# Kernel tuning notes

Measured on AMD Instinct MI355X. Metric: run time of the kernel, lower is better.

Reference implementation:

```python
import jax, jax.numpy as jnp
import numpy as np

STUDENT_TEMP = 0.1
CENTER_MOMENTUM = 0.9
N_CROPS = 8
GLOBAL_CROPS = 2
TOPK = 8
WARMUP_TEACHER_TEMP = 0.04
TEACHER_TEMP = 0.07
WARMUP_EPOCHS = 30
NEPOCHS = 100
B = 256          # per-crop batch
D = 8192         # out_dim


def setup_inputs() -> dict:
    key = jax.random.key(0)
    k1, k2, k3, k4 = jax.random.split(key, 4)
    return {
        "student_output": jax.random.normal(k1, (N_CROPS * B, D), jnp.float32),
        "teacher_output": jax.random.normal(k2, (GLOBAL_CROPS * B, D), jnp.float32),
        "predictor_table": 0.02 * jax.random.normal(k3, (D, D), jnp.float32),
        "center": 0.1 * jax.random.normal(k4, (1, D), jnp.float32),
        "epoch": 35,
    }


def reference(student_output, teacher_output, predictor_table, center, epoch):
    # teacher temperature schedule (static, epoch is a Python int)
    temps = np.concatenate([
        np.linspace(WARMUP_TEACHER_TEMP, TEACHER_TEMP, WARMUP_EPOCHS),
        np.ones(NEPOCHS - WARMUP_EPOCHS) * TEACHER_TEMP,
    ])
    temp = float(temps[epoch])

    # student/teacher softmaxes, chunked per crop
    student_probs = jax.nn.softmax(student_output / STUDENT_TEMP, axis=-1)
    s_chunks = jnp.split(student_probs, N_CROPS, axis=0)          # n_crops x [B, D]
    teacher_probs = jax.nn.softmax((teacher_output - center) / temp, axis=-1)
    t_chunks = jnp.split(teacher_probs, GLOBAL_CROPS, axis=0)     # global_crops x [B, D]

    # pairwise topk-weighted cross entropy
    total_loss = jnp.float32(0.0)
    n_loss_terms = 0
    for iq in range(GLOBAL_CROPS):
        for v in range(N_CROPS):
            if v <= iq:
                continue
            s = t_chunks[iq]                                       # [B, D] teacher probs
            f = s_chunks[v]                                        # [B, D] student probs
            p, indices = jax.lax.top_k(s, TOPK)                    # [B, K]
            p = p / jnp.sum(p, axis=-1, keepdims=True)
            pred = predictor_table[indices] / STUDENT_TEMP         # [B, K, D] gather
            logp = jax.nn.log_softmax(pred, axis=-1)               # [B, K, D]
            # -sum_k sum_d p[b,k] * f[b,d] * logp[b,k,d]  (outer-product weighting)
            loss_b = -jnp.einsum('bk,bd,bkd->b', p, f, logp)
            total_loss = total_loss + loss_b.mean()
            n_loss_terms += 1
    total_loss = total_loss / n_loss_terms

    # EMA center update (no-grad in original; world_size = 1)
    t_ng = jax.lax.stop_gradient(teacher_output)
    batch_center = jnp.mean(t_ng, axis=0, keepdims=True)           # [1, D]
    new_center = center * CENTER_MOMENTUM + batch_center * (1.0 - CENTER_MOMENTUM)

    log_sm_center = jax.nn.log_softmax(center, axis=-1)
    true_entropy = jnp.sum(jax.nn.softmax(center, axis=-1) * log_sm_center, axis=-1)
    entropy = jnp.sum(jax.nn.softmax(batch_center, axis=-1) * log_sm_center, axis=-1)

    return (total_loss, entropy, true_entropy, new_center)
```

## Files before the change

### kernel.cpp

```cpp
#include <hip/hip_runtime.h>
#include <hip/hip_bf16.h>
#include <math.h>

#define D 8192
#define NT 256

__device__ __forceinline__ float wave_sum(float v) {
    #pragma unroll
    for (int o = 32; o > 0; o >>= 1) v += __shfl_xor(v, o, 64);
    return v;
}

__global__ __launch_bounds__(NT) void k_topk(
    const float* __restrict__ teacher, const float* __restrict__ center,
    const int* __restrict__ epoch_p,
    int* __restrict__ idx_ws, float* __restrict__ p_ws, float* __restrict__ out)
{
    const int row = blockIdx.x;
    const int t = threadIdx.x;
    const int lane = t & 63, w = t >> 6;
    __shared__ float svv[8][4];
    __shared__ int   sii[8][4];

    if (row == 0 && t == 0) out[0] = 0.f;

    const int e = epoch_p[0];
    const float temp = (e < 30) ? (0.04f + 0.03f * (float)e / 29.0f) : 0.07f;

    float z[32];
    const float* trow = teacher + (size_t)row * D;
    #pragma unroll
    for (int i = 0; i < 8; ++i) {
        const int d = i * 1024 + t * 4;
        float4 tv = *(const float4*)(trow + d);
        float4 cv = *(const float4*)(center + d);
        z[i*4+0] = tv.x - cv.x; z[i*4+1] = tv.y - cv.y;
        z[i*4+2] = tv.z - cv.z; z[i*4+3] = tv.w - cv.w;
    }

    float mvl = -INFINITY; int mil = 0;
    #pragma unroll
    for (int i = 0; i < 32; ++i)
        if (z[i] > mvl) { mvl = z[i]; mil = i; }

    float topv[8]; int topd[8];
    #pragma unroll 1
    for (int k = 0; k < 8; ++k) {
        float mv = mvl;
        int md = ((mil >> 2) << 10) + t * 4 + (mil & 3);
        #pragma unroll
        for (int o = 32; o > 0; o >>= 1) {
            float ov = __shfl_xor(mv, o, 64);
            int   od = __shfl_xor(md, o, 64);
            if (ov > mv) { mv = ov; md = od; }
        }
        if (lane == 0) { svv[k][w] = mv; sii[k][w] = md; }
        __syncthreads();
        float gv = svv[k][0]; int gd = sii[k][0];
        #pragma unroll
        for (int j = 1; j < 4; ++j)
            if (svv[k][j] > gv) { gv = svv[k][j]; gd = sii[k][j]; }
        topv[k] = gv; topd[k] = gd;
        if (((gd & 1023) >> 2) == t) {
            z[((gd >> 10) << 2) | (gd & 3)] = -INFINITY;
            mvl = -INFINITY; mil = 0;
            #pragma unroll
            for (int i = 0; i < 32; ++i)
                if (z[i] > mvl) { mvl = z[i]; mil = i; }
        }
    }

    if (t == 0) {
        float wgt[8]; float norm = 0.f;
        #pragma unroll
        for (int k = 0; k < 8; ++k) { wgt[k] = __expf((topv[k] - topv[0]) / temp); norm += wgt[k]; }
        const float invn = 1.0f / norm;
        #pragma unroll
        for (int k = 0; k < 8; ++k) {
            p_ws[row * 8 + k] = wgt[k] * invn;
            idx_ws[row * 8 + k] = topd[k];
        }
    }
}

__global__ __launch_bounds__(NT) void k_gather_colsum(
    const float* __restrict__ pred, const int* __restrict__ idx_ws,
    const float* __restrict__ p_ws, const float* __restrict__ teacher,
    float* __restrict__ g_ws, float* __restrict__ part_lse, float* __restrict__ part)
{
    const int bid = blockIdx.x;
    const int t = threadIdx.x;

    if (bid < 128) {
        const int rc = bid >> 3, dc = bid & 7;
        const int d0 = dc * 1024 + t * 4;
        const float* base = teacher + (size_t)rc * 32 * D + d0;
        float4 acc = make_float4(0.f, 0.f, 0.f, 0.f);
        #pragma unroll 4
        for (int r = 0; r < 32; ++r) {
            float4 x = *(const float4*)(base + (size_t)r * D);
            acc.x += x.x; acc.y += x.y; acc.z += x.z; acc.w += x.w;
        }
        *(float4*)(part + (size_t)rc * D + d0) = acc;
        return;
    }

    const int gb  = bid - 128;
    const int row = gb >> 2;
    const int ch  = gb & 3;
    const int lane = t & 63, w = t >> 6;
    const int d0 = ch * 2048 + t * 4;
    __shared__ float sred[4][8];

    int jk[8]; float pk[8];
    #pragma unroll
    for (int k = 0; k < 8; ++k) {
        jk[k] = idx_ws[row * 8 + k];
        pk[k] = p_ws[row * 8 + k];
    }

    float4 a0 = make_float4(0.f,0.f,0.f,0.f), a1 = make_float4(0.f,0.f,0.f,0.f);
    float se[8];
    #pragma unroll
    for (int k = 0; k < 8; ++k) {
        const float* prow = pred + (size_t)jk[k] * D;
        float4 x0 = *(const float4*)(prow + d0);
        float4 x1 = *(const float4*)(prow + d0 + 1024);
        se[k] = __expf(x0.x*10.f) + __expf(x0.y*10.f) + __expf(x0.z*10.f) + __expf(x0.w*10.f)
              + __expf(x1.x*10.f) + __expf(x1.y*10.f) + __expf(x1.z*10.f) + __expf(x1.w*10.f);
        const float p = pk[k];
        a0.x += p*x0.x; a0.y += p*x0.y; a0.z += p*x0.z; a0.w += p*x0.w;
        a1.x += p*x1.x; a1.y += p*x1.y; a1.z += p*x1.z; a1.w += p*x1.w;
    }
    float* grow = g_ws + (size_t)row * D;
    *(float4*)(grow + d0)        = a0;
    *(float4*)(grow + d0 + 1024) = a1;

    #pragma unroll
    for (int k = 0; k < 8; ++k) se[k] = wave_sum(se[k]);
    if (lane == 0) {
        #pragma unroll
        for (int k = 0; k < 8; ++k) sred[w][k] = se[k];
    }
    __syncthreads();
    if (t < 8)
        part_lse[(size_t)gb * 8 + t] =
            sred[0][t] + sred[1][t] + sred[2][t] + sred[3][t];
}

__global__ __launch_bounds__(NT) void k_main(
    const float* __restrict__ student, const float* __restrict__ g_ws,
    const float* __restrict__ p_ws, const float* __restrict__ part_lse,
    const float* __restrict__ part, const float* __restrict__ center,
    float* __restrict__ out)
{
    const int bid = blockIdx.x;
    const int t = threadIdx.x;
    const int lane = t & 63, w = t >> 6;

    if (bid < 2) {
        __shared__ float sm4[4];
        const int r = (bid << 8) | t;
        float c = 0.f;
        #pragma unroll
        for (int k = 0; k < 8; ++k) {
            float s = part_lse[(size_t)(r*4+0)*8+k] + part_lse[(size_t)(r*4+1)*8+k]
                    + part_lse[(size_t)(r*4+2)*8+k] + part_lse[(size_t)(r*4+3)*8+k];
            c += p_ws[r * 8 + k] * __logf(s);
        }
        const float wgt = (bid == 0) ? 7.0f : 6.0f;
        float vv = wave_sum(c * wgt * (1.0f / 3328.0f));
        if (lane == 0) sm4[w] = vv;
        __syncthreads();
        if (t == 0) atomicAdd(out, sm4[0] + sm4[1] + sm4[2] + sm4[3]);
        return;
    }

    if (bid == 2) {
        __shared__ float sm4[4];
        float c[32], bc[32];
        #pragma unroll
        for (int i = 0; i < 8; ++i) {
            const int d = i * 1024 + t * 4;
            float4 cv = *(const float4*)(center + d);
            float4 s = make_float4(0.f, 0.f, 0.f, 0.f);
            for (int rc = 0; rc < 16; ++rc) {
                float4 p = *(const float4*)(part + (size_t)rc * D + d);
                s.x += p.x; s.y += p.y; s.z += p.z; s.w += p.w;
            }
            const float sc = 1.0f / 512.0f;
            bc[i*4+0] = s.x * sc; bc[i*4+1] = s.y * sc;
            bc[i*4+2] = s.z * sc; bc[i*4+3] = s.w * sc;
            c[i*4+0] = cv.x; c[i*4+1] = cv.y; c[i*4+2] = cv.z; c[i*4+3] = cv.w;
            out[3 + d + 0] = cv.x * 0.9f + bc[i*4+0] * 0.1f;
            out[3 + d + 1] = cv.y * 0.9f + bc[i*4+1] * 0.1f;
            out[3 + d + 2] = cv.z * 0.9f + bc[i*4+2] * 0.1f;
            out[3 + d + 3] = cv.w * 0.9f + bc[i*4+3] * 0.1f;
        }

        float mc = -INFINITY, mb = -INFINITY;
        #pragma unroll
        for (int i = 0; i < 32; ++i) { mc = fmaxf(mc, c[i]); mb = fmaxf(mb, bc[i]); }
        #pragma unroll
        for (int o = 32; o > 0; o >>= 1) {
            mc = fmaxf(mc, __shfl_xor(mc, o, 64));
            mb = fmaxf(mb, __shfl_xor(mb, o, 64));
        }
        if (lane == 0) sm4[w] = mc;
        __syncthreads();
        mc = fmaxf(fmaxf(sm4[0], sm4[1]), fmaxf(sm4[2], sm4[3]));
        __syncthreads();
        if (lane == 0) sm4[w] = mb;
        __syncthreads();
        mb = fmaxf(fmaxf(sm4[0], sm4[1]), fmaxf(sm4[2], sm4[3]));
        __syncthreads();

        float zc = 0.f, zb = 0.f;
        #pragma unroll
        for (int i = 0; i < 32; ++i) { zc += __expf(c[i] - mc); zb += __expf(bc[i] - mb); }
        zc = wave_sum(zc); zb = wave_sum(zb);
        if (lane == 0) sm4[w] = zc;
        __syncthreads();
        zc = sm4[0] + sm4[1] + sm4[2] + sm4[3];
        __syncthreads();
        if (lane == 0) sm4[w] = zb;
        __syncthreads();
        zb = sm4[0] + sm4[1] + sm4[2] + sm4[3];
        __syncthreads();
        const float lnZc = __logf(zc);

        float te = 0.f, en = 0.f;
        #pragma unroll
        for (int i = 0; i < 32; ++i) {
            const float lsm = c[i] - mc - lnZc;
            te += __expf(c[i] - mc) * lsm;
            en += __expf(bc[i] - mb) * lsm;
        }
        te = wave_sum(te); en = wave_sum(en);
        if (lane == 0) sm4[w] = te;
        __syncthreads();
        te = sm4[0] + sm4[1] + sm4[2] + sm4[3];
        __syncthreads();
        if (lane == 0) sm4[w] = en;
        __syncthreads();
        en = sm4[0] + sm4[1] + sm4[2] + sm4[3];
        if (t == 0) {
            out[1] = en / zb;
            out[2] = te / zc;
        }
        return;
    }

    __shared__ float sred3[4][3];
    const int row = 253 + bid;
    const int v = row >> 8;
    const int b = row & 255;

    float y[32];
    const float* srow = student + (size_t)row * D;
    #pragma unroll
    for (int i = 0; i < 8; ++i) {
        float4 x = *(const float4*)(srow + i * 1024 + t * 4);
        y[i*4+0] = __expf(x.x * 10.f); y[i*4+1] = __expf(x.y * 10.f);
        y[i*4+2] = __expf(x.z * 10.f); y[i*4+3] = __expf(x.w * 10.f);
    }
    float zs = 0.f;
    #pragma unroll
    for (int i = 0; i < 32; ++i) zs += y[i];

    const float* g0 = g_ws + (size_t)b * D;
    const float* g1 = g_ws + (size_t)(256 + b) * D;
    float a0 = 0.f, a1 = 0.f;
    #pragma unroll
    for (int i = 0; i < 8; ++i) {
        float4 gg = *(const float4*)(g0 + i * 1024 + t * 4);
        a0 += y[i*4+0]*gg.x + y[i*4+1]*gg.y + y[i*4+2]*gg.z + y[i*4+3]*gg.w;
    }
    if (v >= 2) {
        #pragma unroll
        for (int i = 0; i < 8; ++i) {
            float4 gg = *(const float4*)(g1 + i * 1024 + t * 4);
            a1 += y[i*4+0]*gg.x + y[i*4+1]*gg.y + y[i*4+2]*gg.z + y[i*4+3]*gg.w;
        }
    }
    zs = wave_sum(zs); a0 = wave_sum(a0); a1 = wave_sum(a1);
    if (lane == 0) { sred3[w][0] = zs; sred3[w][1] = a0; sred3[w][2] = a1; }
    __syncthreads();
    if (t == 0) {
        const float Z  = sred3[0][0] + sred3[1][0] + sred3[2][0] + sred3[3][0];
        const float A0 = sred3[0][1] + sred3[1][1] + sred3[2][1] + sred3[3][1];
        const float A1 = sred3[0][2] + sred3[1][2] + sred3[2][2] + sred3[3][2];
        const float invZ = 1.0f / Z;
        float term = -10.f * A0 * invZ;
        if (v >= 2) term += -10.f * A1 * invZ;
        atomicAdd(out, term * (1.0f / 3328.0f));
    }
}

extern "C" void kernel_launch(void* const* d_in, const int* in_sizes, int n_in,
                              void* d_out, int out_size, void* d_ws, size_t ws_size,
                              hipStream_t stream) {
    const float* student = (const float*)d_in[0];
    const float* teacher = (const float*)d_in[1];
    const float* pred    = (const float*)d_in[2];
    const float* center  = (const float*)d_in[3];
    const int*   epoch   = (const int*)d_in[4];
    float* out = (float*)d_out;

    float* g_ws     = (float*)d_ws;
    float* part     = g_ws + (size_t)512 * D;
    int*   idx_ws   = (int*)(part + (size_t)16 * D);
    float* p_ws     = (float*)(idx_ws + 512 * 8);
    float* part_lse = p_ws + 512 * 8;

    k_topk<<<512, NT, 0, stream>>>(teacher, center, epoch, idx_ws, p_ws, out);
    k_gather_colsum<<<2176, NT, 0, stream>>>(pred, idx_ws, p_ws, teacher,
                                             g_ws, part_lse, part);
    k_main<<<1795, NT, 0, stream>>>(student, g_ws, p_ws, part_lse, part, center, out);
}
```

Measured before the change: 76.99 us.

## Regroup student loss blocks by batch index to reuse teacher-weighted rows

The student cross-entropy stage now launches one block per (batch index, D-quarter) that processes all seven student crops for that batch index. This lets the two g_ws rows be loaded once and reused across crops instead of being re-read per crop row. Partial sums go to a new workspace and are reduced by an extra small finalize kernel. The gather kernel's block order is also swapped so the column-sum blocks come last. The cost is an additional kernel launch and more register pressure from the seven per-crop accumulators.

```diff
diff --git a/kernel.cpp b/kernel.cpp
--- a/kernel.cpp
+++ b/kernel.cpp
@@ -91,8 +91,9 @@
     const int bid = blockIdx.x;
     const int t = threadIdx.x;
 
-    if (bid < 128) {
-        const int rc = bid >> 3, dc = bid & 7;
+    if (bid >= 2048) {
+        const int cb = bid - 2048;
+        const int rc = cb >> 3, dc = cb & 7;
         const int d0 = dc * 1024 + t * 4;
         const float* base = teacher + (size_t)rc * 32 * D + d0;
         float4 acc = make_float4(0.f, 0.f, 0.f, 0.f);
@@ -105,9 +106,8 @@
         return;
     }
 
-    const int gb  = bid - 128;
-    const int row = gb >> 2;
-    const int ch  = gb & 3;
+    const int row = bid >> 2;
+    const int ch  = bid & 3;
     const int lane = t & 63, w = t >> 6;
     const int d0 = ch * 2048 + t * 4;
     __shared__ float sred[4][8];
@@ -144,7 +144,7 @@
     }
     __syncthreads();
     if (t < 8)
-        part_lse[(size_t)gb * 8 + t] =
+        part_lse[(size_t)bid * 8 + t] =
             sred[0][t] + sred[1][t] + sred[2][t] + sred[3][t];
 }
 
@@ -152,7 +152,7 @@
     const float* __restrict__ student, const float* __restrict__ g_ws,
     const float* __restrict__ p_ws, const float* __restrict__ part_lse,
     const float* __restrict__ part, const float* __restrict__ center,
-    float* __restrict__ out)
+    float* __restrict__ ps_ws, float* __restrict__ out)
 {
     const int bid = blockIdx.x;
     const int t = threadIdx.x;
@@ -251,50 +251,80 @@
         return;
     }
 
-    __shared__ float sred3[4][3];
-    const int row = 253 + bid;
-    const int v = row >> 8;
-    const int b = row & 255;
-
-    float y[32];
-    const float* srow = student + (size_t)row * D;
-    #pragma unroll
-    for (int i = 0; i < 8; ++i) {
-        float4 x = *(const float4*)(srow + i * 1024 + t * 4);
-        y[i*4+0] = __expf(x.x * 10.f); y[i*4+1] = __expf(x.y * 10.f);
-        y[i*4+2] = __expf(x.z * 10.f); y[i*4+3] = __expf(x.w * 10.f);
-    }
-    float zs = 0.f;
-    #pragma unroll
-    for (int i = 0; i < 32; ++i) zs += y[i];
-
-    const float* g0 = g_ws + (size_t)b * D;
-    const float* g1 = g_ws + (size_t)(256 + b) * D;
-    float a0 = 0.f, a1 = 0.f;
-    #pragma unroll
-    for (int i = 0; i < 8; ++i) {
-        float4 gg = *(const float4*)(g0 + i * 1024 + t * 4);
-        a0 += y[i*4+0]*gg.x + y[i*4+1]*gg.y + y[i*4+2]*gg.z + y[i*4+3]*gg.w;
-    }
-    if (v >= 2) {
-        #pragma unroll
-        for (int i = 0; i < 8; ++i) {
-            float4 gg = *(const float4*)(g1 + i * 1024 + t * 4);
-            a1 += y[i*4+0]*gg.x + y[i*4+1]*gg.y + y[i*4+2]*gg.z + y[i*4+3]*gg.w;
-        }
-    }
-    zs = wave_sum(zs); a0 = wave_sum(a0); a1 = wave_sum(a1);
-    if (lane == 0) { sred3[w][0] = zs; sred3[w][1] = a0; sred3[w][2] = a1; }
+    __shared__ float sred21[4][21];
+    const int sb = bid - 3;
+    const int b = sb >> 2, ch = sb & 3;
+    const int d0 = ch * 2048 + t * 4;
+
+    const float* g0p = g_ws + (size_t)b * D + d0;
+    const float* g1p = g_ws + (size_t)(256 + b) * D + d0;
+    const float4 g0a = *(const float4*)(g0p);
+    const float4 g0b = *(const float4*)(g0p + 1024);
+    const float4 g1a = *(const float4*)(g1p);
+    const float4 g1b = *(const float4*)(g1p + 1024);
+
+    float accZ[7], accA0[7], accA1[7];
+    #pragma unroll
+    for (int vi = 0; vi < 7; ++vi) { accZ[vi] = 0.f; accA0[vi] = 0.f; accA1[vi] = 0.f; }
+
+    #pragma unroll
+    for (int vi = 0; vi < 7; ++vi) {
+        const int row = 256 * (vi + 1) + b;
+        const float* sp = student + (size_t)row * D + d0;
+        float4 x0 = *(const float4*)(sp);
+        float4 x1 = *(const float4*)(sp + 1024);
+        float y0 = __expf(x0.x*10.f), y1 = __expf(x0.y*10.f);
+        float y2 = __expf(x0.z*10.f), y3 = __expf(x0.w*10.f);
+        float y4 = __expf(x1.x*10.f), y5 = __expf(x1.y*10.f);
+        float y6 = __expf(x1.z*10.f), y7 = __expf(x1.w*10.f);
+        accZ[vi]  = y0+y1+y2+y3+y4+y5+y6+y7;
+        accA0[vi] = y0*g0a.x + y1*g0a.y + y2*g0a.z + y3*g0a.w
+                  + y4*g0b.x + y5*g0b.y + y6*g0b.z + y7*g0b.w;
+        accA1[vi] = y0*g1a.x + y1*g1a.y + y2*g1a.z + y3*g1a.w
+                  + y4*g1b.x + y5*g1b.y + y6*g1b.z + y7*g1b.w;
+    }
+
+    #pragma unroll
+    for (int vi = 0; vi < 7; ++vi) {
+        accZ[vi]  = wave_sum(accZ[vi]);
+        accA0[vi] = wave_sum(accA0[vi]);
+        accA1[vi] = wave_sum(accA1[vi]);
+    }
+    if (lane == 0) {
+        #pragma unroll
+        for (int vi = 0; vi < 7; ++vi) {
+            sred21[w][vi*3+0] = accZ[vi];
+            sred21[w][vi*3+1] = accA0[vi];
+            sred21[w][vi*3+2] = accA1[vi];
+        }
+    }
     __syncthreads();
-    if (t == 0) {
-        const float Z  = sred3[0][0] + sred3[1][0] + sred3[2][0] + sred3[3][0];
-        const float A0 = sred3[0][1] + sred3[1][1] + sred3[2][1] + sred3[3][1];
-        const float A1 = sred3[0][2] + sred3[1][2] + sred3[2][2] + sred3[3][2];
-        const float invZ = 1.0f / Z;
-        float term = -10.f * A0 * invZ;
-        if (v >= 2) term += -10.f * A1 * invZ;
-        atomicAdd(out, term * (1.0f / 3328.0f));
-    }
+    if (t < 21)
+        ps_ws[(size_t)sb * 24 + t] =
+            sred21[0][t] + sred21[1][t] + sred21[2][t] + sred21[3][t];
+}
+
+__global__ __launch_bounds__(NT) void k_sfinal(
+    const float* __restrict__ ps_ws, float* __restrict__ out)
+{
+    const int t = threadIdx.x;
+    const int lane = t & 63, w = t >> 6;
+    __shared__ float sm4[4];
+    const int g = blockIdx.x * NT + t;
+    const int vi = g >> 8;
+    const int b  = g & 255;
+
+    float Z = 0.f, A0 = 0.f, A1 = 0.f;
+    #pragma unroll
+    for (int ch = 0; ch < 4; ++ch) {
+        const float* p = ps_ws + (size_t)(b * 4 + ch) * 24 + vi * 3;
+        Z += p[0]; A0 += p[1]; A1 += p[2];
+    }
+    float term = -10.f * (A0 + ((vi >= 1) ? A1 : 0.f)) / Z;
+    float vv = wave_sum(term * (1.0f / 3328.0f));
+    if (lane == 0) sm4[w] = vv;
+    __syncthreads();
+    if (t == 0) atomicAdd(out, sm4[0] + sm4[1] + sm4[2] + sm4[3]);
 }
 
 extern "C" void kernel_launch(void* const* d_in, const int* in_sizes, int n_in,
@@ -312,9 +342,12 @@
     int*   idx_ws   = (int*)(part + (size_t)16 * D);
     float* p_ws     = (float*)(idx_ws + 512 * 8);
     float* part_lse = p_ws + 512 * 8;
+    float* ps_ws    = part_lse + 2048 * 8;
 
     k_topk<<<512, NT, 0, stream>>>(teacher, center, epoch, idx_ws, p_ws, out);
     k_gather_colsum<<<2176, NT, 0, stream>>>(pred, idx_ws, p_ws, teacher,
                                              g_ws, part_lse, part);
-    k_main<<<1795, NT, 0, stream>>>(student, g_ws, p_ws, part_lse, part, center, out);
-}
+    k_main<<<1027, NT, 0, stream>>>(student, g_ws, p_ws, part_lse, part, center,
+                                    ps_ws, out);
+    k_sfinal<<<7, NT, 0, stream>>>(ps_ws, out);
+}
```

Measured after the change: 71.46 us. 7.2% less time.
